# Optimization experiments

Hardware: AMD Instinct MI355X
Metric: run time of the kernel (lower is better)

The kernel has to match this reference:

```python
import jax, jax.numpy as jnp
import numpy as np
import math

D_MODEL = 192
D_STATE = 16
D_CONV = 3
D_INNER = 2 * D_MODEL
DT_RANK = math.ceil(D_MODEL / 16)  # 12
BATCH, HH, WW = 8, 48, 48
DT_MIN, DT_MAX = 1e-3, 1e-1
EPS = 1e-5


def setup_inputs() -> dict:
    key = jax.random.key(0)
    ks = jax.random.split(key, 10)
    x = jax.random.normal(ks[0], (BATCH, D_MODEL, HH, WW), dtype=jnp.float32)
    in_proj_w = jax.random.normal(ks[1], (2 * D_INNER, D_MODEL), dtype=jnp.float32) * (D_MODEL ** -0.5)
    conv_w = jax.random.normal(ks[2], (D_INNER, 1, D_CONV, D_CONV), dtype=jnp.float32) * (1.0 / 3.0)
    conv_b = jnp.zeros((D_INNER,), dtype=jnp.float32)
    x_proj_w = jax.random.normal(ks[3], (DT_RANK + 2 * D_STATE, D_INNER), dtype=jnp.float32) * (D_INNER ** -0.5)
    dt_std = DT_RANK ** -0.5
    dt_proj_w = jax.random.uniform(ks[4], (D_INNER, DT_RANK), dtype=jnp.float32, minval=-dt_std, maxval=dt_std)
    u = jax.random.uniform(ks[5], (D_INNER,), dtype=jnp.float32)
    dt_proj_b = jnp.exp(u * (math.log(DT_MAX) - math.log(DT_MIN)) + math.log(DT_MIN))
    A_log = jnp.log(jnp.tile(jnp.arange(1, D_STATE + 1, dtype=jnp.float32)[None, :], (D_INNER, 1)))
    D_param = jnp.ones((D_INNER,), dtype=jnp.float32)
    ln_g = jnp.ones((D_INNER,), dtype=jnp.float32)
    ln_b = jnp.zeros((D_INNER,), dtype=jnp.float32)
    out_proj_w = jax.random.normal(ks[6], (D_MODEL, D_INNER), dtype=jnp.float32) * (D_INNER ** -0.5)
    fuse_w = jax.random.normal(ks[7], (D_MODEL, D_MODEL, 1, 1), dtype=jnp.float32) * (D_MODEL ** -0.5)
    fuse_b = jnp.zeros((D_MODEL,), dtype=jnp.float32)
    return dict(x=x, in_proj_w=in_proj_w, conv_w=conv_w, conv_b=conv_b,
                x_proj_w=x_proj_w, dt_proj_w=dt_proj_w, dt_proj_b=dt_proj_b,
                A_log=A_log, D_param=D_param, ln_g=ln_g, ln_b=ln_b,
                out_proj_w=out_proj_w, fuse_w=fuse_w, fuse_b=fuse_b)


def _silu(v):
    return v * jax.nn.sigmoid(v)


def _selective_scan(u, delta, A, Bp, Cp, D_param):
    # u, delta: [B, L, Di]; A: [Di, Ds]; Bp, Cp: [B, L, Ds]; D_param: [Di]
    deltaA = jnp.exp(delta[..., None] * A)                    # [B, L, Di, Ds]
    deltaBu = (delta * u)[..., None] * Bp[:, :, None, :]      # [B, L, Di, Ds]
    a_seq = jnp.moveaxis(deltaA, 1, 0)                        # [L, B, Di, Ds]
    b_seq = jnp.moveaxis(deltaBu, 1, 0)
    c_seq = jnp.moveaxis(Cp, 1, 0)                            # [L, B, Ds]

    def step(h, abc):
        a_t, b_t, c_t = abc
        h = a_t * h + b_t                                     # [B, Di, Ds]
        y = jnp.einsum('bds,bs->bd', h, c_t)                  # [B, Di]
        return h, y

    h0 = jnp.zeros(u.shape[:1] + (u.shape[2], A.shape[1]), dtype=u.dtype)
    _, ys = jax.lax.scan(step, h0, (a_seq, b_seq, c_seq))     # ys: [L, B, Di]
    return jnp.moveaxis(ys, 0, 1) + u * D_param               # [B, L, Di]


def reference(x, in_proj_w, conv_w, conv_b, x_proj_w, dt_proj_w, dt_proj_b,
              A_log, D_param, ln_g, ln_b, out_proj_w, fuse_w, fuse_b):
    Bn, C, H, W = x.shape
    L = H * W
    x_hwc = jnp.transpose(x, (0, 2, 3, 1))                    # [B, H, W, C]
    xz = jnp.einsum('bhwc,oc->bhwo', x_hwc, in_proj_w)        # [B, H, W, 2*Di]
    xin, z = jnp.split(xz, 2, axis=-1)
    xin_c = jnp.transpose(xin, (0, 3, 1, 2))                  # [B, Di, H, W]
    conv = jax.lax.conv_general_dilated(
        xin_c, conv_w, window_strides=(1, 1), padding='SAME',
        feature_group_count=D_INNER,
        dimension_numbers=('NCHW', 'OIHW', 'NCHW')) + conv_b[None, :, None, None]
    xact = _silu(conv)
    x_flat = jnp.transpose(xact.reshape(Bn, D_INNER, L), (0, 2, 1))  # [B, L, Di]
    xp = jnp.einsum('bld,od->blo', x_flat, x_proj_w)          # [B, L, dt_rank+2*Ds]
    dt_low = xp[..., :DT_RANK]
    Bp = xp[..., DT_RANK:DT_RANK + D_STATE]                   # [B, L, Ds]
    Cp = xp[..., DT_RANK + D_STATE:]                          # [B, L, Ds]
    dt = jnp.einsum('blr,dr->bld', dt_low, dt_proj_w)         # [B, L, Di]
    delta = jax.nn.softplus(dt + dt_proj_b)
    A = -jnp.exp(A_log)
    y = _selective_scan(x_flat, delta, A, Bp, Cp, D_param)    # [B, L, Di]
    out = y.reshape(Bn, H, W, D_INNER)
    mu = out.mean(axis=-1, keepdims=True)
    var = out.var(axis=-1, keepdims=True)
    out = (out - mu) * jax.lax.rsqrt(var + EPS) * ln_g + ln_b
    out = out * _silu(z)
    out = jnp.einsum('bhwd,od->bhwo', out, out_proj_w)        # [B, H, W, d_model]
    out_c = jnp.transpose(out, (0, 3, 1, 2))                  # [B, d_model, H, W]
    fused = jnp.einsum('bchw,oc->bohw', out_c, fuse_w[:, :, 0, 0]) + fuse_b[None, :, None, None]
    m = fused.mean(axis=(2, 3), keepdims=True)
    v = fused.var(axis=(2, 3), keepdims=True)
    normed = (fused - m) * jax.lax.rsqrt(v + EPS)             # InstanceNorm2d, no affine
    return x + normed
```

## Files before the change

kernel.cpp:

```cpp
#include <hip/hip_runtime.h>
#include <math.h>

#define B_ 8
#define DM 192
#define DI 384
#define DS 16
#define DTR 12
#define NP 44
#define H_ 48
#define W_ 48
#define L_ (H_*W_)
#define NR (B_*L_)
#define EPS_ 1e-5f
#define CH 96
#define CL 24

typedef unsigned int u32;
typedef unsigned short u16;
typedef _Float16 f16;
typedef _Float16 f16x8 __attribute__((ext_vector_type(8)));
typedef float f32x4 __attribute__((ext_vector_type(4)));

__device__ __forceinline__ u16 f2h(float f) {
  f16 h = (f16)f;
  return __builtin_bit_cast(u16, h);
}
__device__ __forceinline__ float h2f(u16 u) {
  f16 h = __builtin_bit_cast(f16, u);
  return (float)h;
}
__device__ __forceinline__ u32 pack2h(float a, float b) {
  return (u32)f2h(a) | ((u32)f2h(b) << 16);
}

__device__ __forceinline__ void rpowers(float r, float* pw) {
  float r2 = r*r, r4 = r2*r2, r8 = r4*r4;
  pw[0]=r;         pw[1]=r2;        pw[2]=r2*r;      pw[3]=r4;
  pw[4]=r4*r;      pw[5]=r4*r2;     pw[6]=r4*pw[2];  pw[7]=r8;
  pw[8]=r8*r;      pw[9]=r8*r2;     pw[10]=r8*pw[2]; pw[11]=r8*r4;
  pw[12]=r8*pw[4]; pw[13]=r8*pw[5]; pw[14]=r8*pw[6]; pw[15]=r8*r8;
}

__global__ __launch_bounds__(384) void k_prep(const float* __restrict__ x,
                                              const float* __restrict__ in_w,
                                              const float* __restrict__ xproj_w,
                                              const float* __restrict__ outp_w,
                                              const float* __restrict__ fuse_w,
                                              u16* __restrict__ xT,
                                              u16* __restrict__ Wi,
                                              u16* __restrict__ Wx,
                                              u16* __restrict__ Wc) {
  __shared__ float tile[32][33];
  const int bid = blockIdx.x;
  const int tid = threadIdx.x;
  if (bid < 192) {
    const int o = bid, c = tid;
    float acc = 0.f;
    #pragma unroll 4
    for (int n = 0; n < DM; ++n)
      acc += fuse_w[o*DM + n] * outp_w[(size_t)n*DI + c];
    Wc[(size_t)o*DI + c] = f2h(acc);
  } else if (bid < 3648) {
    const int t = bid - 192;
    const int c0 = (t % 6)*32, l0 = ((t/6) % 72)*32, b = t/(6*72);
    for (int e = tid; e < 1024; e += 384) {
      int ci = e >> 5, li = e & 31;
      tile[ci][li] = x[((size_t)b*DM + c0+ci)*L_ + l0+li];
    }
    __syncthreads();
    for (int e = tid; e < 1024; e += 384) {
      int li = e >> 5, ci = e & 31;
      xT[((size_t)b*L_ + l0+li)*DM + c0+ci] = f2h(tile[ci][li]);
    }
  } else if (bid < 3744) {
    const int q = (bid - 3648)*384 + tid;
    const float4 v = *(const float4*)(in_w + (size_t)q*4);
    u32* dst = (u32*)(Wi + (size_t)q*4);
    dst[0] = pack2h(v.x, v.y);
    dst[1] = pack2h(v.z, v.w);
  } else {
    const int q = (bid - 3744)*384 + tid;
    const float4 v = *(const float4*)(xproj_w + (size_t)q*4);
    u32* dst = (u32*)(Wx + (size_t)q*4);
    dst[0] = pack2h(v.x, v.y);
    dst[1] = pack2h(v.z, v.w);
  }
}

template<int TM, int TN, int KT, int MODE>
__global__ __launch_bounds__(256) void k_tgemm(const u16* __restrict__ A, int lda,
                                               const u16* __restrict__ W, int N,
                                               void* __restrict__ outA,
                                               void* __restrict__ outB,
                                               const float* __restrict__ bias) {
  constexpr int K = KT*32;
  constexpr int WM = TM/2, WN = TN/2;
  constexpr int MT = WM/16, NT = WN/16;
  __shared__ u16 As[TM*72];
  __shared__ u16 Bs[TN*72];
  const int tid = threadIdx.x;
  const int gx = gridDim.x;
  const int nwg = gx * gridDim.y;
  int bid = blockIdx.y * gx + blockIdx.x;
  if ((nwg & 7) == 0) {
    const int qq = nwg >> 3;
    bid = (bid & 7) * qq + (bid >> 3);
  }
  const int n0 = (bid % gx) * TN;
  const int r0 = (bid / gx) * TM;
  const int lane = tid & 63;
  const int wave = tid >> 6;
  const int wm = (wave & 1) * WM, wn = (wave >> 1) * WN;
  const int lrow = lane & 15, lq = lane >> 4;
  f32x4 acc[MT][NT] = {};
  for (int k0 = 0; k0 < K; k0 += 64) {
    for (int i = tid; i < TM*8; i += 256) {
      int row = i >> 3, seg = i & 7;
      f16x8 v = *(const f16x8*)(A + (size_t)(r0+row)*lda + k0 + seg*8);
      *(f16x8*)&As[row*72 + seg*8] = v;
    }
    for (int i = tid; i < TN*8; i += 256) {
      int row = i >> 3, seg = i & 7;
      int n = n0 + row;
      f16x8 v = {};
      if (n < N) v = *(const f16x8*)(W + (size_t)n*K + k0 + seg*8);
      *(f16x8*)&Bs[row*72 + seg*8] = v;
    }
    __syncthreads();
    #pragma unroll
    for (int kk = 0; kk < 2; ++kk) {
      f16x8 af[MT], bfr[NT];
      #pragma unroll
      for (int t = 0; t < MT; ++t)
        af[t] = *(const f16x8*)&As[(wm + t*16 + lrow)*72 + kk*32 + lq*8];
      #pragma unroll
      for (int t = 0; t < NT; ++t)
        bfr[t] = *(const f16x8*)&Bs[(wn + t*16 + lrow)*72 + kk*32 + lq*8];
      #pragma unroll
      for (int tm = 0; tm < MT; ++tm)
        #pragma unroll
        for (int tn = 0; tn < NT; ++tn)
          acc[tm][tn] = __builtin_amdgcn_mfma_f32_16x16x32_f16(af[tm], bfr[tn], acc[tm][tn], 0, 0, 0);
    }
    __syncthreads();
  }
  #pragma unroll
  for (int tm = 0; tm < MT; ++tm) {
    const int mb = r0 + wm + tm*16 + lq*4;
    #pragma unroll
    for (int tn = 0; tn < NT; ++tn) {
      const int col = n0 + wn + tn*16 + lrow;
      if (MODE == 0) {
        if (col < DI) {
          u16* o = (u16*)outA;
          #pragma unroll
          for (int i = 0; i < 4; ++i) o[(size_t)(mb+i)*DI + col] = f2h(acc[tm][tn][i]);
        } else {
          u16* o = (u16*)outB;
          #pragma unroll
          for (int i = 0; i < 4; ++i) o[(size_t)(mb+i)*DI + (col-DI)] = f2h(acc[tm][tn][i]);
        }
      }
    }
  }
}

__global__ __launch_bounds__(256) void k_conv_silu(const u16* __restrict__ xin,
                                                   const float* __restrict__ cw,
                                                   const float* __restrict__ cb,
                                                   u16* __restrict__ xact) {
  int idx = blockIdx.x*256 + threadIdx.x;
  int cg = idx % 48;
  int pos = idx / 48;
  int w = pos % W_; int h = (pos / W_) % H_; int b = pos / L_;
  int c8 = cg*8;
  float wv[72];
  const float4* wp = (const float4*)(cw + (size_t)c8*9);
  #pragma unroll
  for (int i = 0; i < 18; ++i) {
    float4 t4 = wp[i];
    wv[i*4]=t4.x; wv[i*4+1]=t4.y; wv[i*4+2]=t4.z; wv[i*4+3]=t4.w;
  }
  float acc[8];
  {
    const float4* cbp = (const float4*)(cb + c8);
    float4 b0 = cbp[0], b1 = cbp[1];
    acc[0]=b0.x; acc[1]=b0.y; acc[2]=b0.z; acc[3]=b0.w;
    acc[4]=b1.x; acc[5]=b1.y; acc[6]=b1.z; acc[7]=b1.w;
  }
  #pragma unroll
  for (int dh = -1; dh <= 1; ++dh) {
    int hh = h + dh; if (hh < 0 || hh >= H_) continue;
    #pragma unroll
    for (int dw = -1; dw <= 1; ++dw) {
      int w2 = w + dw; if (w2 < 0 || w2 >= W_) continue;
      int j = (dh+1)*3 + (dw+1);
      const uint4 q = *(const uint4*)(xin + ((size_t)b*L_ + hh*W_ + w2)*DI + c8);
      float v[8];
      v[0]=h2f((u16)(q.x & 0xFFFF)); v[1]=h2f((u16)(q.x >> 16));
      v[2]=h2f((u16)(q.y & 0xFFFF)); v[3]=h2f((u16)(q.y >> 16));
      v[4]=h2f((u16)(q.z & 0xFFFF)); v[5]=h2f((u16)(q.z >> 16));
      v[6]=h2f((u16)(q.w & 0xFFFF)); v[7]=h2f((u16)(q.w >> 16));
      #pragma unroll
      for (int i = 0; i < 8; ++i) acc[i] += v[i]*wv[i*9+j];
    }
  }
  u32 res[4];
  #pragma unroll
  for (int i = 0; i < 4; ++i) {
    float a0 = acc[2*i],   s0 = a0 / (1.f + __expf(-a0));
    float a1 = acc[2*i+1], s1 = a1 / (1.f + __expf(-a1));
    res[i] = pack2h(s0, s1);
  }
  *(uint4*)(xact + (size_t)pos*DI + c8) = make_uint4(res[0], res[1], res[2], res[3]);
}


__global__ __launch_bounds__(384) void k_scan_A(const u16* __restrict__ u,
                                                const u16* __restrict__ Wx,
                                                const float* __restrict__ dtw,
                                                const float* __restrict__ dtb,
                                                const float* __restrict__ Dp,
                                                u16* __restrict__ yl,
                                                u16* __restrict__ Pc,
                                                float* __restrict__ Cb,
                                                u16* __restrict__ Pb,
                                                u16* __restrict__ hLb) {
  __shared__ u16 tl[32*392];
  __shared__ float xps[CL*48];
  const int tid = threadIdx.x;
  const int b = blockIdx.x, c = blockIdx.y;
  const size_t rbase = (size_t)b*L_ + (size_t)c*CL;
  for (int i = tid; i < CL*48; i += 384) {
    int r = i / 48, seg = i % 48;
    *(f16x8*)&tl[r*392 + seg*8] = *(const f16x8*)(u + (rbase + r)*DI + seg*8);
  }
  __syncthreads();
  {
    const int lane = tid & 63, wave = tid >> 6;
    const int lrow = lane & 15, lq = lane >> 4;
    const int mi = wave / 3, ni = wave % 3;
    const int n = ni*16 + lrow;
    f32x4 a2 = {};
    #pragma unroll 4
    for (int ks = 0; ks < 12; ++ks) {
      f16x8 af = *(const f16x8*)&tl[(mi*16 + lrow)*392 + ks*32 + lq*8];
      f16x8 bf = {};
      if (n < NP) bf = *(const f16x8*)(Wx + (size_t)n*DI + ks*32 + lq*8);
      a2 = __builtin_amdgcn_mfma_f32_16x16x32_f16(af, bf, a2, 0, 0, 0);
    }
    #pragma unroll
    for (int i = 0; i < 4; ++i) {
      const int j = mi*16 + lq*4 + i;
      if (j < CL && n < NP) xps[j*48 + n] = a2[i];
    }
  }
  __syncthreads();
  Cb[rbase*16 + tid] = xps[(tid >> 4)*48 + 28 + (tid & 15)];
  float wr[12];
  #pragma unroll
  for (int k = 0; k < 12; ++k) wr[k] = dtw[tid*DTR + k];
  const float bd = dtb[tid];
  const float Dpar = Dp[tid];
  float h[16] = {};
  float sdlt = 0.f;
  float P = 1.f;
  for (int j = 0; j < CL; ++j) {
    float uu = h2f(tl[j*392 + tid]);
    const float* xr = &xps[j*48];
    float dt = bd;
    #pragma unroll
    for (int k = 0; k < 12; ++k) dt += xr[k]*wr[k];
    float dlt = (dt > 20.f) ? dt : __logf(1.f + __expf(dt));
    sdlt += dlt;
    float du = dlt*uu;
    float r = __expf(-dlt);
    float pw[16]; rpowers(r, pw);
    float yv = uu * Dpar;
    #pragma unroll
    for (int s = 0; s < 16; ++s) {
      h[s] = pw[s]*h[s] + du*xr[12+s];
      yv += h[s]*xr[28+s];
    }
    P *= r;
    yl[(rbase+j)*DI + tid] = f2h(yv);
    Pc[(rbase+j)*DI + tid] = f2h(P);
  }
  float rt = __expf(-sdlt);
  const size_t o = (((size_t)c*B_ + b)*DI + tid)*DS;
  u32 pk[8];
  {
    float pw[16]; rpowers(rt, pw);
    #pragma unroll
    for (int k = 0; k < 8; ++k) pk[k] = pack2h(pw[2*k], pw[2*k+1]);
  }
  *(uint4*)&Pb[o]   = make_uint4(pk[0], pk[1], pk[2], pk[3]);
  *(uint4*)&Pb[o+8] = make_uint4(pk[4], pk[5], pk[6], pk[7]);
  #pragma unroll
  for (int k = 0; k < 8; ++k) pk[k] = pack2h(h[2*k], h[2*k+1]);
  *(uint4*)&hLb[o]   = make_uint4(pk[0], pk[1], pk[2], pk[3]);
  *(uint4*)&hLb[o+8] = make_uint4(pk[4], pk[5], pk[6], pk[7]);
}

__global__ __launch_bounds__(256) void k_scan_B(const u16* __restrict__ Pb,
                                                const u16* __restrict__ hLb,
                                                u16* __restrict__ Sb) {
  const size_t gid = (size_t)blockIdx.x*256 + threadIdx.x;
  float run = 0.f;
  #pragma unroll 8
  for (int c = 0; c < CH; ++c) {
    size_t o = (size_t)c*(B_*DI*DS) + gid;
    Sb[o] = f2h(run);
    run = h2f(Pb[o])*run + h2f(hLb[o]);
  }
}

__global__ __launch_bounds__(384) void k_scan_C(const u16* __restrict__ yl,
                                                const u16* __restrict__ Pc,
                                                const float* __restrict__ Cb,
                                                const u16* __restrict__ Sb,
                                                const u16* __restrict__ z,
                                                const float* __restrict__ g,
                                                const float* __restrict__ be,
                                                const u16* __restrict__ Wc,
                                                const float* __restrict__ fb,
                                                u16* __restrict__ fused) {
  __shared__ float arena[CL*388];
  __shared__ float smv[CL][2];
  __shared__ float Cs[CL*16];
  float* sy = arena;
  u16*   tl = (u16*)arena;
  const int tid = threadIdx.x;
  const int b = blockIdx.x, c = blockIdx.y;
  const size_t rbase = (size_t)b*L_ + (size_t)c*CL;
  Cs[tid] = Cb[rbase*16 + tid];
  const float gd = g[tid], bed = be[tid];
  float hi[16];
  {
    const size_t o = (((size_t)c*B_ + b)*DI + tid)*DS;
    uint4 q0 = *(const uint4*)&Sb[o];
    uint4 q1 = *(const uint4*)&Sb[o+8];
    const u32 qs[8] = {q0.x,q0.y,q0.z,q0.w,q1.x,q1.y,q1.z,q1.w};
    #pragma unroll
    for (int k = 0; k < 8; ++k) {
      hi[2*k]   = h2f((u16)(qs[k] & 0xFFFF));
      hi[2*k+1] = h2f((u16)(qs[k] >> 16));
    }
  }
  __syncthreads();
  #pragma unroll 4
  for (int j = 0; j < CL; ++j) {
    float y = h2f(yl[(rbase+j)*DI + tid]);
    float P = h2f(Pc[(rbase+j)*DI + tid]);
    float t = Cs[j*16 + 15]*hi[15];
    #pragma unroll
    for (int s = 14; s >= 0; --s) t = Cs[j*16 + s]*hi[s] + P*t;
    sy[j*388 + tid] = y + P*t;
  }
  __syncthreads();
  {
    const int row = tid >> 4, p = tid & 15;
    float s = 0.f, q = 0.f;
    #pragma unroll
    for (int k = 0; k < 24; ++k) {
      float v = sy[row*388 + p + 16*k];
      s += v; q += v*v;
    }
    #pragma unroll
    for (int m = 1; m < 16; m <<= 1) { s += __shfl_xor(s, m); q += __shfl_xor(q, m); }
    if (p == 0) {
      float mu = s * (1.f/DI);
      float var = q * (1.f/DI) - mu*mu;
      smv[row][0] = mu;
      smv[row][1] = rsqrtf(var + EPS_);
    }
  }
  __syncthreads();
  u32 treg[12];
  #pragma unroll
  for (int jp = 0; jp < 12; ++jp) {
    float tv[2];
    #pragma unroll
    for (int hl = 0; hl < 2; ++hl) {
      const int j = jp*2 + hl;
      float mu = smv[j][0], rstd = smv[j][1];
      float yv = sy[j*388 + tid];
      float zz = h2f(z[(rbase+j)*DI + tid]);
      float sz = zz / (1.f + __expf(-zz));
      tv[hl] = ((yv - mu)*rstd*gd + bed) * sz;
    }
    treg[jp] = pack2h(tv[0], tv[1]);
  }
  __syncthreads();
  #pragma unroll
  for (int jp = 0; jp < 12; ++jp) {
    tl[(jp*2  )*392 + tid] = (u16)(treg[jp] & 0xFFFF);
    tl[(jp*2+1)*392 + tid] = (u16)(treg[jp] >> 16);
  }
  #pragma unroll
  for (int i = 0; i < 8; ++i) tl[(24+i)*392 + tid] = 0;
  __syncthreads();
  {
    const int lane = tid & 63, wave = tid >> 6;
    const int lrow = lane & 15, lq = lane >> 4;
    const int o0 = wave * 32;
    f32x4 a2[2][2] = {};
    #pragma unroll 4
    for (int ks = 0; ks < 12; ++ks) {
      f16x8 af[2], bf[2];
      #pragma unroll
      for (int t = 0; t < 2; ++t)
        af[t] = *(const f16x8*)&tl[(t*16 + lrow)*392 + ks*32 + lq*8];
      #pragma unroll
      for (int t = 0; t < 2; ++t)
        bf[t] = *(const f16x8*)(Wc + (size_t)(o0 + t*16 + lrow)*DI + ks*32 + lq*8);
      #pragma unroll
      for (int tm = 0; tm < 2; ++tm)
        #pragma unroll
        for (int tn = 0; tn < 2; ++tn)
          a2[tm][tn] = __builtin_amdgcn_mfma_f32_16x16x32_f16(af[tm], bf[tn], a2[tm][tn], 0, 0, 0);
    }
    #pragma unroll
    for (int tm = 0; tm < 2; ++tm) {
      const int l = tm*16 + lq*4;
      if (l < CL) {
        #pragma unroll
        for (int tn = 0; tn < 2; ++tn) {
          const int o = o0 + tn*16 + lrow;
          const float bv = fb[o];
          u16 r4[4];
          #pragma unroll
          for (int i = 0; i < 4; ++i) r4[i] = f2h(a2[tm][tn][i] + bv);
          *(uint2*)(fused + ((size_t)b*DM + o)*L_ + (size_t)c*CL + l) =
              make_uint2((u32)r4[0] | ((u32)r4[1] << 16),
                         (u32)r4[2] | ((u32)r4[3] << 16));
        }
      }
    }
  }
}

__global__ __launch_bounds__(256) void k_inorm(const u16* __restrict__ fused,
                                               const float* __restrict__ x,
                                               float* __restrict__ out) {
  const int bo = blockIdx.x;
  const int tid = threadIdx.x;
  const u16* row = fused + (size_t)bo*L_;
  float s = 0.f, q = 0.f;
  float vr[9];
  #pragma unroll
  for (int k = 0; k < 9; ++k) {
    float v = h2f(row[tid + k*256]);
    vr[k] = v; s += v; q += v*v;
  }
  #pragma unroll
  for (int m = 1; m < 64; m <<= 1) { s += __shfl_xor(s, m); q += __shfl_xor(q, m); }
  __shared__ float ps[4], pq[4];
  if ((tid&63)==0) { ps[tid>>6]=s; pq[tid>>6]=q; }
  __syncthreads();
  float S = ps[0]+ps[1]+ps[2]+ps[3];
  float Q = pq[0]+pq[1]+pq[2]+pq[3];
  float mu = S/(float)L_;
  float var = Q/(float)L_ - mu*mu;
  float rstd = rsqrtf(var + EPS_);
  #pragma unroll
  for (int k = 0; k < 9; ++k) {
    size_t idx = (size_t)bo*L_ + tid + k*256;
    out[idx] = x[idx] + (vr[k]-mu)*rstd;
  }
}

extern "C" void kernel_launch(void* const* d_in, const int* in_sizes, int n_in,
                              void* d_out, int out_size, void* d_ws, size_t ws_size,
                              hipStream_t stream) {
  const float* x       = (const float*)d_in[0];
  const float* in_w    = (const float*)d_in[1];
  const float* conv_w  = (const float*)d_in[2];
  const float* conv_b  = (const float*)d_in[3];
  const float* xproj_w = (const float*)d_in[4];
  const float* dt_w    = (const float*)d_in[5];
  const float* dt_b    = (const float*)d_in[6];
  const float* D_par   = (const float*)d_in[8];
  const float* ln_g    = (const float*)d_in[9];
  const float* ln_bb   = (const float*)d_in[10];
  const float* outp_w  = (const float*)d_in[11];
  const float* fuse_w  = (const float*)d_in[12];
  const float* fuse_b  = (const float*)d_in[13];
  float* out = (float*)d_out;

  float* ws = (float*)d_ws;
  const size_t o_xT    = 0;
  const size_t o_xin   = 1769472;
  const size_t o_z     = 5308416;
  const size_t o_xact  = 8847360;
  const size_t o_xp    = 12386304;
  const size_t o_Wc    = 13197312;
  const size_t o_Wi    = 13234176;
  const size_t o_Wx    = 13307904;
  const size_t o_Pb    = 13316352;
  const size_t o_hL    = 15675648;
  const size_t o_Sb    = 18034944;

  u16*   xT    = (u16*)(ws + o_xT);
  u16*   xin   = (u16*)(ws + o_xin);
  u16*   zb    = (u16*)(ws + o_z);
  u16*   xact  = (u16*)(ws + o_xact);
  float* Cb    = ws + o_xp;
  u16*   Wc    = (u16*)(ws + o_Wc);
  u16*   Wi    = (u16*)(ws + o_Wi);
  u16*   Wx    = (u16*)(ws + o_Wx);
  u16*   Pb    = (u16*)(ws + o_Pb);
  u16*   hLb   = (u16*)(ws + o_hL);
  u16*   Sb    = (u16*)(ws + o_Sb);
  u16*   yl    = xact;
  u16*   Pc    = (u16*)(ws + 0);
  u16*   fused = (u16*)(ws + o_Pb);

  k_prep<<<3755, 384, 0, stream>>>(x, in_w, xproj_w, outp_w, fuse_w, xT, Wi, Wx, Wc);
  k_tgemm<128,128,6,0><<<dim3(6,144), 256, 0, stream>>>(xT, DM, Wi, 2*DI, xin, zb, nullptr);
  k_conv_silu<<<NR*48/256, 256, 0, stream>>>(xin, conv_w, conv_b, xact);
  k_scan_A<<<dim3(B_, CH), 384, 0, stream>>>(xact, Wx, dt_w, dt_b, D_par, yl, Pc, Cb, Pb, hLb);
  k_scan_B<<<(B_*DI*DS)/256, 256, 0, stream>>>(Pb, hLb, Sb);
  k_scan_C<<<dim3(B_, CH), 384, 0, stream>>>(yl, Pc, Cb, Sb, zb, ln_g, ln_bb, Wc, fuse_b, fused);
  k_inorm<<<B_*DM, 256, 0, stream>>>(fused, x, out);
}
```

Baseline: 235.9 us.

## Fuse x transpose into input-projection GEMM and simplify scan decay math

Removes the separate transpose-and-convert stage for x from the prep kernel and instead loads fp32 x directly in channel-major layout inside the input-projection GEMM, converting to fp16 while scattering it into shared memory. This drops a full round trip of the transposed activation through global memory and shrinks the prep launch. In the scan kernel, exp(-softplus(dt)) is computed as 1/(1+exp(dt)), which reuses one exponential, and the final chunk decay reuses the running product P instead of summing deltas. The scattered 2-byte shared-memory stores in the GEMM may cause bank conflicts, and the GEMM re-reads x once per N-tile column.

Measured after the change: 244.2 us. +3.5%, slower.

```diff
diff --git a/kernel.cpp b/kernel.cpp
--- a/kernel.cpp
+++ b/kernel.cpp
@@ -41,16 +41,13 @@
   pw[12]=r8*pw[4]; pw[13]=r8*pw[5]; pw[14]=r8*pw[6]; pw[15]=r8*r8;
 }
 
-__global__ __launch_bounds__(384) void k_prep(const float* __restrict__ x,
-                                              const float* __restrict__ in_w,
+__global__ __launch_bounds__(384) void k_prep(const float* __restrict__ in_w,
                                               const float* __restrict__ xproj_w,
                                               const float* __restrict__ outp_w,
                                               const float* __restrict__ fuse_w,
-                                              u16* __restrict__ xT,
                                               u16* __restrict__ Wi,
                                               u16* __restrict__ Wx,
                                               u16* __restrict__ Wc) {
-  __shared__ float tile[32][33];
   const int bid = blockIdx.x;
   const int tid = threadIdx.x;
   if (bid < 192) {
@@ -60,26 +57,14 @@
     for (int n = 0; n < DM; ++n)
       acc += fuse_w[o*DM + n] * outp_w[(size_t)n*DI + c];
     Wc[(size_t)o*DI + c] = f2h(acc);
-  } else if (bid < 3648) {
-    const int t = bid - 192;
-    const int c0 = (t % 6)*32, l0 = ((t/6) % 72)*32, b = t/(6*72);
-    for (int e = tid; e < 1024; e += 384) {
-      int ci = e >> 5, li = e & 31;
-      tile[ci][li] = x[((size_t)b*DM + c0+ci)*L_ + l0+li];
-    }
-    __syncthreads();
-    for (int e = tid; e < 1024; e += 384) {
-      int li = e >> 5, ci = e & 31;
-      xT[((size_t)b*L_ + l0+li)*DM + c0+ci] = f2h(tile[ci][li]);
-    }
-  } else if (bid < 3744) {
-    const int q = (bid - 3648)*384 + tid;
+  } else if (bid < 288) {
+    const int q = (bid - 192)*384 + tid;
     const float4 v = *(const float4*)(in_w + (size_t)q*4);
     u32* dst = (u32*)(Wi + (size_t)q*4);
     dst[0] = pack2h(v.x, v.y);
     dst[1] = pack2h(v.z, v.w);
   } else {
-    const int q = (bid - 3744)*384 + tid;
+    const int q = (bid - 288)*384 + tid;
     const float4 v = *(const float4*)(xproj_w + (size_t)q*4);
     u32* dst = (u32*)(Wx + (size_t)q*4);
     dst[0] = pack2h(v.x, v.y);
@@ -87,79 +72,72 @@
   }
 }
 
-template<int TM, int TN, int KT, int MODE>
-__global__ __launch_bounds__(256) void k_tgemm(const u16* __restrict__ A, int lda,
-                                               const u16* __restrict__ W, int N,
-                                               void* __restrict__ outA,
-                                               void* __restrict__ outB,
-                                               const float* __restrict__ bias) {
-  constexpr int K = KT*32;
-  constexpr int WM = TM/2, WN = TN/2;
-  constexpr int MT = WM/16, NT = WN/16;
-  __shared__ u16 As[TM*72];
-  __shared__ u16 Bs[TN*72];
+__global__ __launch_bounds__(256) void k_gemm_in(const float* __restrict__ x,
+                                                 const u16* __restrict__ W,
+                                                 u16* __restrict__ outA,
+                                                 u16* __restrict__ outB) {
+  __shared__ u16 As[128*72];
+  __shared__ u16 Bs[128*72];
   const int tid = threadIdx.x;
   const int gx = gridDim.x;
   const int nwg = gx * gridDim.y;
   int bid = blockIdx.y * gx + blockIdx.x;
-  if ((nwg & 7) == 0) {
+  {
     const int qq = nwg >> 3;
     bid = (bid & 7) * qq + (bid >> 3);
   }
-  const int n0 = (bid % gx) * TN;
-  const int r0 = (bid / gx) * TM;
+  const int n0 = (bid % gx) * 128;
+  const int r0 = (bid / gx) * 128;
+  const int b  = r0 / L_, l0 = r0 % L_;
   const int lane = tid & 63;
   const int wave = tid >> 6;
-  const int wm = (wave & 1) * WM, wn = (wave >> 1) * WN;
-  const int lrow = lane & 15, lq = lane >> 4;
-  f32x4 acc[MT][NT] = {};
-  for (int k0 = 0; k0 < K; k0 += 64) {
-    for (int i = tid; i < TM*8; i += 256) {
+  const int wm = (wave & 1) * 64, wn = (wave >> 1) * 64;
+  const int lrow = lane & 15, lq4 = lane >> 4;
+  f32x4 acc[4][4] = {};
+  for (int k0 = 0; k0 < 192; k0 += 64) {
+    for (int i = tid; i < 64*32; i += 256) {
+      const int c = i & 63, lq = i >> 6;
+      const float4 v = *(const float4*)(x + ((size_t)b*DM + k0 + c)*L_ + l0 + lq*4);
+      As[(lq*4+0)*72 + c] = f2h(v.x);
+      As[(lq*4+1)*72 + c] = f2h(v.y);
+      As[(lq*4+2)*72 + c] = f2h(v.z);
+      As[(lq*4+3)*72 + c] = f2h(v.w);
+    }
+    for (int i = tid; i < 128*8; i += 256) {
       int row = i >> 3, seg = i & 7;
-      f16x8 v = *(const f16x8*)(A + (size_t)(r0+row)*lda + k0 + seg*8);
-      *(f16x8*)&As[row*72 + seg*8] = v;
-    }
-    for (int i = tid; i < TN*8; i += 256) {
-      int row = i >> 3, seg = i & 7;
-      int n = n0 + row;
-      f16x8 v = {};
-      if (n < N) v = *(const f16x8*)(W + (size_t)n*K + k0 + seg*8);
+      f16x8 v = *(const f16x8*)(W + (size_t)(n0+row)*192 + k0 + seg*8);
       *(f16x8*)&Bs[row*72 + seg*8] = v;
     }
     __syncthreads();
     #pragma unroll
     for (int kk = 0; kk < 2; ++kk) {
-      f16x8 af[MT], bfr[NT];
-      #pragma unroll
-      for (int t = 0; t < MT; ++t)
-        af[t] = *(const f16x8*)&As[(wm + t*16 + lrow)*72 + kk*32 + lq*8];
-      #pragma unroll
-      for (int t = 0; t < NT; ++t)
-        bfr[t] = *(const f16x8*)&Bs[(wn + t*16 + lrow)*72 + kk*32 + lq*8];
-      #pragma unroll
-      for (int tm = 0; tm < MT; ++tm)
+      f16x8 af[4], bfr[4];
+      #pragma unroll
+      for (int t = 0; t < 4; ++t)
+        af[t] = *(const f16x8*)&As[(wm + t*16 + lrow)*72 + kk*32 + lq4*8];
+      #pragma unroll
+      for (int t = 0; t < 4; ++t)
+        bfr[t] = *(const f16x8*)&Bs[(wn + t*16 + lrow)*72 + kk*32 + lq4*8];
+      #pragma unroll
+      for (int tm = 0; tm < 4; ++tm)
         #pragma unroll
-        for (int tn = 0; tn < NT; ++tn)
+        for (int tn = 0; tn < 4; ++tn)
           acc[tm][tn] = __builtin_amdgcn_mfma_f32_16x16x32_f16(af[tm], bfr[tn], acc[tm][tn], 0, 0, 0);
     }
     __syncthreads();
   }
   #pragma unroll
-  for (int tm = 0; tm < MT; ++tm) {
-    const int mb = r0 + wm + tm*16 + lq*4;
-    #pragma unroll
-    for (int tn = 0; tn < NT; ++tn) {
+  for (int tm = 0; tm < 4; ++tm) {
+    const int mb = r0 + wm + tm*16 + lq4*4;
+    #pragma unroll
+    for (int tn = 0; tn < 4; ++tn) {
       const int col = n0 + wn + tn*16 + lrow;
-      if (MODE == 0) {
-        if (col < DI) {
-          u16* o = (u16*)outA;
-          #pragma unroll
-          for (int i = 0; i < 4; ++i) o[(size_t)(mb+i)*DI + col] = f2h(acc[tm][tn][i]);
-        } else {
-          u16* o = (u16*)outB;
-          #pragma unroll
-          for (int i = 0; i < 4; ++i) o[(size_t)(mb+i)*DI + (col-DI)] = f2h(acc[tm][tn][i]);
-        }
+      if (col < DI) {
+        #pragma unroll
+        for (int i = 0; i < 4; ++i) outA[(size_t)(mb+i)*DI + col] = f2h(acc[tm][tn][i]);
+      } else {
+        #pragma unroll
+        for (int i = 0; i < 4; ++i) outB[(size_t)(mb+i)*DI + (col-DI)] = f2h(acc[tm][tn][i]);
       }
     }
   }
@@ -263,7 +241,6 @@
   const float bd = dtb[tid];
   const float Dpar = Dp[tid];
   float h[16] = {};
-  float sdlt = 0.f;
   float P = 1.f;
   for (int j = 0; j < CL; ++j) {
     float uu = h2f(tl[j*392 + tid]);
@@ -271,10 +248,10 @@
     float dt = bd;
     #pragma unroll
     for (int k = 0; k < 12; ++k) dt += xr[k]*wr[k];
-    float dlt = (dt > 20.f) ? dt : __logf(1.f + __expf(dt));
-    sdlt += dlt;
+    float e = __expf(dt);
+    float dlt = (dt > 20.f) ? dt : __logf(1.f + e);
+    float r = __builtin_amdgcn_rcpf(1.f + e);
     float du = dlt*uu;
-    float r = __expf(-dlt);
     float pw[16]; rpowers(r, pw);
     float yv = uu * Dpar;
     #pragma unroll
@@ -286,7 +263,7 @@
     yl[(rbase+j)*DI + tid] = f2h(yv);
     Pc[(rbase+j)*DI + tid] = f2h(P);
   }
-  float rt = __expf(-sdlt);
+  const float rt = P;
   const size_t o = (((size_t)c*B_ + b)*DI + tid)*DS;
   u32 pk[8];
   {
@@ -489,7 +466,6 @@
   float* out = (float*)d_out;
 
   float* ws = (float*)d_ws;
-  const size_t o_xT    = 0;
   const size_t o_xin   = 1769472;
   const size_t o_z     = 5308416;
   const size_t o_xact  = 8847360;
@@ -501,7 +477,6 @@
   const size_t o_hL    = 15675648;
   const size_t o_Sb    = 18034944;
 
-  u16*   xT    = (u16*)(ws + o_xT);
   u16*   xin   = (u16*)(ws + o_xin);
   u16*   zb    = (u16*)(ws + o_z);
   u16*   xact  = (u16*)(ws + o_xact);
@@ -516,8 +491,8 @@
   u16*   Pc    = (u16*)(ws + 0);
   u16*   fused = (u16*)(ws + o_Pb);
 
-  k_prep<<<3755, 384, 0, stream>>>(x, in_w, xproj_w, outp_w, fuse_w, xT, Wi, Wx, Wc);
-  k_tgemm<128,128,6,0><<<dim3(6,144), 256, 0, stream>>>(xT, DM, Wi, 2*DI, xin, zb, nullptr);
+  k_prep<<<299, 384, 0, stream>>>(in_w, xproj_w, outp_w, fuse_w, Wi, Wx, Wc);
+  k_gemm_in<<<dim3(6,144), 256, 0, stream>>>(x, Wi, xin, zb);
   k_conv_silu<<<NR*48/256, 256, 0, stream>>>(xin, conv_w, conv_b, xact);
   k_scan_A<<<dim3(B_, CH), 384, 0, stream>>>(xact, Wx, dt_w, dt_b, D_par, yl, Pc, Cb, Pb, hLb);
   k_scan_B<<<(B_*DI*DS)/256, 256, 0, stream>>>(Pb, hLb, Sb);
```
